# Performance work log

Hardware: AMD Instinct MI355X
Metric: run time of the kernel (lower is better)

## Reference

```python
import jax, jax.numpy as jnp
import numpy as np
import math

N_HEAD = 16
ROPE_BASE = 10000.0


def _rope(xh):
    # xh: [B, H, T, D]; rotate full head dim using half-split (GPT-NeoX style)
    B, H, T, D = xh.shape
    theta = 1.0 / (ROPE_BASE ** (jnp.arange(0, D, 2, dtype=jnp.float32) / D))  # [D/2]
    idx_theta = jnp.arange(T, dtype=jnp.float32)[:, None] * theta[None, :]      # [T, D/2]
    idx_theta2 = jnp.concatenate([idx_theta, idx_theta], axis=1)                 # [T, D]
    cos = jnp.cos(idx_theta2)[None, None]                                        # [1,1,T,D]
    sin = jnp.sin(idx_theta2)[None, None]
    d2 = D // 2
    neg_half = jnp.concatenate([-xh[..., d2:], xh[..., :d2]], axis=-1)
    return xh * cos + neg_half * sin


def setup_inputs() -> dict:
    key = jax.random.key(0)
    k1, k2, k3 = jax.random.split(key, 3)
    B, T, C = 2, 2048, 2048
    x = jax.random.normal(k1, (B, T, C), dtype=jnp.float32)
    w_attn = jax.random.normal(k2, (C, 3 * C), dtype=jnp.float32) * (1.0 / math.sqrt(C))
    w_proj = jax.random.normal(k3, (C, C), dtype=jnp.float32) * (1.0 / math.sqrt(C))
    return {"x": x, "w_attn": w_attn, "w_proj": w_proj}


def reference(x, w_attn, w_proj):
    B, T, C = x.shape
    H = N_HEAD
    D = C // H
    qkv = x @ w_attn                                   # [B,T,3C]
    q, k, v = jnp.split(qkv, 3, axis=-1)
    # [B,T,C] -> [B,H,T,D]
    to_heads = lambda t: t.reshape(B, T, H, D).transpose(0, 2, 1, 3)
    q, k, v = to_heads(q), to_heads(k), to_heads(v)
    q = _rope(q)
    k = _rope(k)
    att = jnp.einsum('bhqd,bhkd->bhqk', q, k) * (1.0 / math.sqrt(D))
    causal = jnp.tril(jnp.ones((T, T), dtype=bool))
    att = jnp.where(causal[None, None], att, -jnp.inf)
    att = jax.nn.softmax(att, axis=-1)
    y = jnp.einsum('bhqk,bhkd->bhqd', att, v)          # [B,H,T,D]
    y = y.transpose(0, 2, 1, 3).reshape(B, T, C)
    return y @ w_proj
```

## Files before the change

kernel.cpp:

```cpp
#include <hip/hip_runtime.h>
#include <hip/hip_bf16.h>
#include <math.h>

typedef __bf16 bf16;
typedef __bf16 bf16x8 __attribute__((ext_vector_type(8)));
typedef float f32x4 __attribute__((ext_vector_type(4)));
typedef float f32x16 __attribute__((ext_vector_type(16)));
typedef unsigned int u32x2 __attribute__((ext_vector_type(2)));
typedef unsigned int u32x4 __attribute__((ext_vector_type(4)));

#define MFMA16(a, b, c) __builtin_amdgcn_mfma_f32_16x16x32_bf16((a), (b), (c), 0, 0, 0)
#define MFMA32(a, b, c) __builtin_amdgcn_mfma_f32_32x32x16_bf16((a), (b), (c), 0, 0, 0)

static constexpr int Bsz = 2, Tsz = 2048, Csz = 2048, Hn = 16, Dh = 128;
static constexpr float ATTN_SCALE = 0.08838834764831845f;

__device__ __forceinline__ void gld16(const void* src, void* dst) {
    __builtin_amdgcn_global_load_lds((__attribute__((address_space(1))) void*)src,
                                     (__attribute__((address_space(3))) void*)dst,
                                     16, 0, 0);
}

__device__ __forceinline__ unsigned cvt_pk_bf16(float lo, float hi) {
    unsigned r;
    asm("v_cvt_pk_bf16_f32 %0, %1, %2" : "=v"(r) : "v"(lo), "v"(hi));
    return r;
}

__device__ __forceinline__ bf16x8 make_pfrag(float p0, float p1, float p2, float p3,
                                             float p4, float p5, float p6, float p7) {
    unsigned a0 = cvt_pk_bf16(p0, p1), a1 = cvt_pk_bf16(p2, p3);
    unsigned b0 = cvt_pk_bf16(p4, p5), b1 = cvt_pk_bf16(p6, p7);
    asm volatile("v_permlane32_swap_b32 %0, %1" : "+v"(a0), "+v"(b0));
    asm volatile("v_permlane32_swap_b32 %0, %1" : "+v"(a1), "+v"(b1));
    u32x4 w = {a0, a1, b0, b1};
    return __builtin_bit_cast(bf16x8, w);
}

__global__ __launch_bounds__(256) void cast_x_kernel(const float* __restrict__ x,
                                                     bf16* __restrict__ o, int n8) {
    int i = blockIdx.x * 256 + threadIdx.x;
    if (i >= n8) return;
    const float4* x4 = (const float4*)x;
    float4 a = x4[2 * i], b = x4[2 * i + 1];
    bf16x8 v;
    v[0] = (bf16)a.x; v[1] = (bf16)a.y; v[2] = (bf16)a.z; v[3] = (bf16)a.w;
    v[4] = (bf16)b.x; v[5] = (bf16)b.y; v[6] = (bf16)b.z; v[7] = (bf16)b.w;
    ((bf16x8*)o)[i] = v;
}

template <typename TIN>
__global__ __launch_bounds__(256) void transpose_cast_kernel(const TIN* __restrict__ in,
                                                             bf16* __restrict__ out,
                                                             int R, int Cc) {
    __shared__ float tile[64][65];
    const int tx = threadIdx.x, ty = threadIdx.y;
    in  += (size_t)blockIdx.z * R * Cc;
    out += (size_t)blockIdx.z * R * Cc;
    const int c0 = blockIdx.x * 64, r0 = blockIdx.y * 64;
#pragma unroll
    for (int j = 0; j < 16; ++j) {
        int rr = ty + j * 4;
        tile[rr][tx] = (float)in[(size_t)(r0 + rr) * Cc + c0 + tx];
    }
    __syncthreads();
#pragma unroll
    for (int j = 0; j < 16; ++j) {
        int cc = ty + j * 4;
        out[(size_t)(c0 + cc) * R + r0 + tx] = (bf16)tile[tx][cc];
    }
}

__global__ __launch_bounds__(256) void cossin_kernel(float2* __restrict__ cs) {
    int idx = blockIdx.x * 256 + threadIdx.x;
    int t = idx >> 6, i = idx & 63;
    float theta = 1.0f / powf(10000.0f, (float)(2 * i) / 128.0f);
    float ang = (float)t * theta;
    cs[idx] = make_float2(cosf(ang), sinf(ang));
}

__global__ __launch_bounds__(512, 2)
void gemm256_qkv(const bf16* __restrict__ A, const bf16* __restrict__ Bt,
                 bf16* __restrict__ Oq, bf16* __restrict__ Ok, bf16* __restrict__ Ov,
                 const float2* __restrict__ cs, int K) {
    __shared__ bf16 sA[2][256 * 64];
    __shared__ bf16 sB[2][256 * 64];
    const int tid = threadIdx.x, lane = tid & 63, wid = tid >> 6;
    const int wm = wid >> 2, wn = wid & 3;
    const int lo16 = lane & 15, hi4 = lane >> 4;

    const int cpx = gridDim.x >> 3;
    const int swz = (blockIdx.x & 7) * cpx + (blockIdx.x >> 3);
    const int by = swz & 15;
    const int bx = swz >> 4;
    const int row0 = by << 8, col0 = bx << 8;

    const int srow = tid >> 3;
    const int swzoff = (((tid & 7) ^ ((tid >> 3) & 7)) << 3);
    const bf16* srcA = A  + (size_t)(row0 + srow) * K + swzoff;
    const bf16* srcB = Bt + (size_t)(col0 + srow) * K + swzoff;
    const size_t K64 = (size_t)K * 64, K128 = (size_t)K * 128;
    char* const ldsA = (char*)&sA[0][0];
    char* const ldsB = (char*)&sB[0][0];
    const int wuo = wid << 10;

    auto issueA0 = [&](int c, int kt) {
        const bf16* s = srcA + (size_t)kt * 64;
        gld16(s,        ldsA + (c << 15) + 0     + wuo);
        gld16(s + K128, ldsA + (c << 15) + 16384 + wuo);
    };
    auto issueA1 = [&](int c, int kt) {
        const bf16* s = srcA + (size_t)kt * 64 + K64;
        gld16(s,        ldsA + (c << 15) + 8192  + wuo);
        gld16(s + K128, ldsA + (c << 15) + 24576 + wuo);
    };
    auto issueBlo = [&](int c, int kt) {
        const bf16* s = srcB + (size_t)kt * 64;
        gld16(s,       ldsB + (c << 15) + 0    + wuo);
        gld16(s + K64, ldsB + (c << 15) + 8192 + wuo);
    };
    auto issueBhi = [&](int c, int kt) {
        const bf16* s = srcB + (size_t)kt * 64 + K128;
        gld16(s,       ldsB + (c << 15) + 16384 + wuo);
        gld16(s + K64, ldsB + (c << 15) + 24576 + wuo);
    };
    auto ldF = [&](const char* buf, int row, int ks) {
        return *(const bf16x8*)(buf + row * 128 + ((((ks << 2) + hi4) ^ (row & 7)) << 4));
    };

    const int arow = (wm << 7) + lo16;
    const int brow = (wn << 4) + lo16;

    f32x4 acc[8][4] = {};
    const int nkt = K >> 6;

    issueBhi(0, 0); issueA1(0, 0); issueA0(0, 0); issueBlo(0, 0);
    if (nkt > 1) {
        issueA0(1, 1); issueBlo(1, 1);
        asm volatile("s_waitcnt vmcnt(4)" ::: "memory");
    } else {
        asm volatile("s_waitcnt vmcnt(0)" ::: "memory");
    }
    __builtin_amdgcn_s_barrier();

    for (int kt = 0; kt < nkt; ++kt) {
        const int c = kt & 1;
        const char* bufA = ldsA + (c << 15);
        const char* bufB = ldsB + (c << 15);
        bf16x8 af[4][2], bq[2][2];
#pragma unroll
        for (int i = 0; i < 4; ++i) {
            af[i][0] = ldF(bufA, arow + (i << 4), 0);
            af[i][1] = ldF(bufA, arow + (i << 4), 1);
        }
#pragma unroll
        for (int j = 0; j < 2; ++j) {
            bq[j][0] = ldF(bufB, brow + (j << 6), 0);
            bq[j][1] = ldF(bufB, brow + (j << 6), 1);
        }
        if (kt + 1 < nkt) issueBhi(c ^ 1, kt + 1);
        __builtin_amdgcn_s_barrier();
        asm volatile("s_waitcnt lgkmcnt(0)" ::: "memory");
        __builtin_amdgcn_sched_barrier(0);
        __builtin_amdgcn_s_setprio(1);
#pragma unroll
        for (int ks = 0; ks < 2; ++ks)
#pragma unroll
            for (int i = 0; i < 4; ++i)
#pragma unroll
                for (int j = 0; j < 2; ++j)
                    acc[i][j] = MFMA16(af[i][ks], bq[j][ks], acc[i][j]);
        __builtin_amdgcn_s_setprio(0);
        __builtin_amdgcn_s_barrier();
#pragma unroll
        for (int j = 0; j < 2; ++j) {
            bq[j][0] = ldF(bufB, brow + ((j + 2) << 6), 0);
            bq[j][1] = ldF(bufB, brow + ((j + 2) << 6), 1);
        }
        if (kt + 1 < nkt) issueA1(c ^ 1, kt + 1);
        __builtin_amdgcn_s_barrier();
        asm volatile("s_waitcnt lgkmcnt(0)" ::: "memory");
        __builtin_amdgcn_sched_barrier(0);
        __builtin_amdgcn_s_setprio(1);
#pragma unroll
        for (int ks = 0; ks < 2; ++ks)
#pragma unroll
            for (int i = 0; i < 4; ++i)
#pragma unroll
                for (int j = 0; j < 2; ++j)
                    acc[i][j + 2] = MFMA16(af[i][ks], bq[j][ks], acc[i][j + 2]);
        __builtin_amdgcn_s_setprio(0);
        __builtin_amdgcn_s_barrier();
#pragma unroll
        for (int i = 0; i < 4; ++i) {
            af[i][0] = ldF(bufA, arow + 64 + (i << 4), 0);
            af[i][1] = ldF(bufA, arow + 64 + (i << 4), 1);
        }
#pragma unroll
        for (int j = 0; j < 2; ++j) {
            bq[j][0] = ldF(bufB, brow + (j << 6), 0);
            bq[j][1] = ldF(bufB, brow + (j << 6), 1);
        }
        if (kt + 2 < nkt) issueA0(c, kt + 2);
        __builtin_amdgcn_s_barrier();
        asm volatile("s_waitcnt lgkmcnt(0)" ::: "memory");
        __builtin_amdgcn_sched_barrier(0);
        __builtin_amdgcn_s_setprio(1);
#pragma unroll
        for (int ks = 0; ks < 2; ++ks)
#pragma unroll
            for (int i = 0; i < 4; ++i)
#pragma unroll
                for (int j = 0; j < 2; ++j)
                    acc[i + 4][j] = MFMA16(af[i][ks], bq[j][ks], acc[i + 4][j]);
        __builtin_amdgcn_s_setprio(0);
        __builtin_amdgcn_s_barrier();
#pragma unroll
        for (int j = 0; j < 2; ++j) {
            bq[j][0] = ldF(bufB, brow + ((j + 2) << 6), 0);
            bq[j][1] = ldF(bufB, brow + ((j + 2) << 6), 1);
        }
        if (kt + 2 < nkt) issueBlo(c, kt + 2);
        __builtin_amdgcn_s_barrier();
        asm volatile("s_waitcnt lgkmcnt(0)" ::: "memory");
        __builtin_amdgcn_sched_barrier(0);
        __builtin_amdgcn_s_setprio(1);
#pragma unroll
        for (int ks = 0; ks < 2; ++ks)
#pragma unroll
            for (int i = 0; i < 4; ++i)
#pragma unroll
                for (int j = 0; j < 2; ++j)
                    acc[i + 4][j + 2] = MFMA16(af[i][ks], bq[j][ks], acc[i + 4][j + 2]);
        __builtin_amdgcn_s_setprio(0);
        if (kt + 2 < nkt) asm volatile("s_waitcnt vmcnt(4)" ::: "memory");
        else              asm volatile("s_waitcnt vmcnt(0)" ::: "memory");
        __builtin_amdgcn_s_barrier();
    }

    const int seg = col0 >> 11;
    const int hb = (col0 >> 7) & 15;
    if (seg < 2) {
        bf16* dst0 = (seg == 0) ? Oq : Ok;
        const float qs = (seg == 0) ? ATTN_SCALE : 1.0f;
        const int d = (wn << 4) + lo16;
#pragma unroll
        for (int mi = 0; mi < 8; ++mi)
#pragma unroll
            for (int r = 0; r < 4; ++r) {
                const int gm = row0 + (wm << 7) + (mi << 4) + (hi4 << 2) + r;
                const int b = gm >> 11, t = gm & 2047;
                const float2 csv = cs[t * 64 + d];
#pragma unroll
                for (int np = 0; np < 2; ++np) {
                    bf16* drow = dst0 + ((((size_t)b * Hn + hb + np) * Tsz + t) << 7);
                    const float vlo = acc[mi][2 * np][r];
                    const float vhi = acc[mi][2 * np + 1][r];
                    drow[d]      = (bf16)((vlo * csv.x - vhi * csv.y) * qs);
                    drow[d + 64] = (bf16)((vhi * csv.x + vlo * csv.y) * qs);
                }
            }
    } else {
        const int d0 = (wn << 4) + lo16;
#pragma unroll
        for (int mi = 0; mi < 8; ++mi)
#pragma unroll
            for (int r = 0; r < 4; ++r) {
                const int gm = row0 + (wm << 7) + (mi << 4) + (hi4 << 2) + r;
                const int b = gm >> 11, t = gm & 2047;
#pragma unroll
                for (int ni = 0; ni < 4; ++ni) {
                    bf16* drow = Ov + ((((size_t)b * Hn + hb + (ni >> 1)) * Tsz + t) << 7);
                    drow[d0 + ((ni & 1) << 6)] = (bf16)acc[mi][ni][r];
                }
            }
    }
}

__global__ __launch_bounds__(256)
void gemm128_bt(const bf16* __restrict__ A, const bf16* __restrict__ Bt,
                float* __restrict__ Cf, int M, int N, int K) {
    __shared__ bf16 sA[128 * 64];
    __shared__ bf16 sB[128 * 64];
    const int tid = threadIdx.x;
    const int lane = tid & 63, wv = tid >> 6;
    const int wr = wv >> 1, wc = wv & 1;
    const int lo16 = lane & 15, hi4 = lane >> 4;
    const int row0 = blockIdx.y << 7, col0 = blockIdx.x << 7;

    f32x4 acc[4][4] = {};

    const int nkt = K >> 6;
    for (int kt = 0; kt < nkt; ++kt) {
        const int kbase = kt << 6;
#pragma unroll
        for (int c = 0; c < 4; ++c) {
            const int o16 = (c << 8) + tid;
            const int row = o16 >> 3, u = o16 & 7;
            const int colel = kbase + ((u ^ (row & 7)) << 3);
            gld16(A  + (size_t)(row0 + row) * K + colel,
                  (char*)sA + (((c << 8) + (wv << 6)) << 4));
            gld16(Bt + (size_t)(col0 + row) * K + colel,
                  (char*)sB + (((c << 8) + (wv << 6)) << 4));
        }
        __syncthreads();
#pragma unroll
        for (int ks = 0; ks < 2; ++ks) {
            bf16x8 af[4], bfv[4];
#pragma unroll
            for (int mi = 0; mi < 4; ++mi) {
                const int ar = (wr << 6) + (mi << 4) + lo16;
                af[mi] = *(const bf16x8*)((const char*)sA + ar * 128 +
                          (((ks << 6) + (hi4 << 4)) ^ ((ar & 7) << 4)));
            }
#pragma unroll
            for (int ni = 0; ni < 4; ++ni) {
                const int bc = (wc << 4) + (ni << 5) + lo16;
                bfv[ni] = *(const bf16x8*)((const char*)sB + bc * 128 +
                           (((ks << 6) + (hi4 << 4)) ^ ((bc & 7) << 4)));
            }
#pragma unroll
            for (int mi = 0; mi < 4; ++mi)
#pragma unroll
                for (int ni = 0; ni < 4; ++ni)
                    acc[mi][ni] = MFMA16(af[mi], bfv[ni], acc[mi][ni]);
        }
        __syncthreads();
    }

#pragma unroll
    for (int mi = 0; mi < 4; ++mi)
#pragma unroll
        for (int r = 0; r < 4; ++r) {
            const int gm = row0 + (wr << 6) + (mi << 4) + (hi4 << 2) + r;
            float* crow = Cf + (size_t)gm * N + col0 + (wc << 4) + lo16;
#pragma unroll
            for (int ni = 0; ni < 4; ++ni)
                crow[ni << 5] = acc[mi][ni][r];
        }
}

__device__ __forceinline__ void stage_tile(const bf16* __restrict__ Kb,
                                           const bf16* __restrict__ Vtb,
                                           bf16* sKc, bf16* sVc, int k0, int tid) {
#pragma unroll
    for (int c = 0; c < 4; ++c) {
        const int off = (c << 12) + (tid << 4);
        const int row = off >> 8, u = (off >> 4) & 15;
        gld16(Kb + (size_t)(k0 + row) * Dh + ((u ^ (row & 7)) << 3), (char*)sKc + off);
        const int dv = off >> 7, uv = (off >> 4) & 7;
        gld16(Vtb + (size_t)dv * Tsz + k0 + ((uv ^ (dv & 7)) << 3), (char*)sVc + off);
    }
}

__global__ __launch_bounds__(256, 2)
void attn_kernel(const bf16* __restrict__ Q, const bf16* __restrict__ K,
                 const bf16* __restrict__ Vt, bf16* __restrict__ Y) {
    __shared__ bf16 sK[2][64 * 128];
    __shared__ bf16 sV[2][128 * 64];
    const int tid = threadIdx.x, lane = tid & 63, wv = tid >> 6;
    const int lo32 = lane & 31, hl = lane >> 5;

    const int i = blockIdx.x;
    const int g = i >> 5;
    const int bh = i & 31;
    const int t = (i < 256) ? (15 - g) : (g - 8);
    const int b = bh >> 4, h = bh & 15;

    const int q0 = t << 7;
    const int q0w = q0 + (wv << 5);
    const int qg = q0w + lo32;

    const bf16* Kb  = K  + (size_t)bh * (Tsz * Dh);
    const bf16* Vtb = Vt + (size_t)bh * (Tsz * Dh);
    const bf16* Qp  = Q  + (size_t)bh * (Tsz * Dh) + (size_t)qg * Dh;

    bf16x8 qf[8];
#pragma unroll
    for (int kc = 0; kc < 8; ++kc)
        qf[kc] = *(const bf16x8*)(Qp + (kc << 4) + (hl << 3));

    float m = -1e30f, lsum = 0.f;
    f32x16 o[4] = {};

    const int nt_block = 2 * t + 2;
    const int nt_warp = ((q0w + 31) >> 6) + 1;

    stage_tile(Kb, Vtb, &sK[0][0], &sV[0][0], 0, tid);

    int cur = 0;
    for (int kt = 0; kt < nt_block; ++kt) {
        __syncthreads();
        if (kt + 1 < nt_block)
            stage_tile(Kb, Vtb, &sK[cur ^ 1][0], &sV[cur ^ 1][0], (kt + 1) << 6, tid);
        if (kt < nt_warp) {
            const int k0 = kt << 6;
            const bf16* kbuf = &sK[cur][0];
            const bf16* vbuf = &sV[cur][0];
            f32x16 s0 = {}, s1 = {};
            const int swk = lo32 & 7;
            __builtin_amdgcn_s_setprio(1);
#pragma unroll
            for (int kc = 0; kc < 8; ++kc) {
                bf16x8 kf0 = *(const bf16x8*)((const char*)kbuf + lo32 * 256 +
                              ((((kc << 1) + hl) ^ swk) << 4));
                s0 = MFMA32(kf0, qf[kc], s0);
                bf16x8 kf1 = *(const bf16x8*)((const char*)kbuf + (32 + lo32) * 256 +
                              ((((kc << 1) + hl) ^ swk) << 4));
                s1 = MFMA32(kf1, qf[kc], s1);
            }
            __builtin_amdgcn_s_setprio(0);

            const bool bnd = (k0 + 63 > q0w);
            if (bnd) {
#pragma unroll
                for (int r = 0; r < 16; ++r) {
                    const int kl = (r & 3) + ((r >> 2) << 3) + (hl << 2);
                    if (k0 + kl > qg)      s0[r] = -1e30f;
                    if (k0 + 32 + kl > qg) s1[r] = -1e30f;
                }
            }
            float pm = s0[0];
#pragma unroll
            for (int r = 1; r < 16; ++r) pm = fmaxf(pm, s0[r]);
#pragma unroll
            for (int r = 0; r < 16; ++r) pm = fmaxf(pm, s1[r]);
            pm = fmaxf(pm, __shfl_xor(pm, 32));

            if (__any(pm > m + 8.0f)) {
                const float mn = fmaxf(m, pm);
                const float sc = __expf(m - mn);
                m = mn;
                lsum *= sc;
#pragma unroll
                for (int db = 0; db < 4; ++db)
#pragma unroll
                    for (int r = 0; r < 16; ++r) o[db][r] *= sc;
            }
            float rs = 0.f;
            if (bnd) {
#pragma unroll
                for (int r = 0; r < 16; ++r) {
                    float e0 = (s0[r] > -1e29f) ? __expf(s0[r] - m) : 0.f;
                    float e1 = (s1[r] > -1e29f) ? __expf(s1[r] - m) : 0.f;
                    s0[r] = e0; s1[r] = e1; rs += e0 + e1;
                }
            } else {
#pragma unroll
                for (int r = 0; r < 16; ++r) {
                    float e0 = __expf(s0[r] - m);
                    float e1 = __expf(s1[r] - m);
                    s0[r] = e0; s1[r] = e1; rs += e0 + e1;
                }
            }
            rs += __shfl_xor(rs, 32);
            lsum += rs;

            bf16x8 pb0 = make_pfrag(s0[0], s0[1], s0[2],  s0[3],  s0[4],  s0[5],  s0[6],  s0[7]);
            bf16x8 pb1 = make_pfrag(s0[8], s0[9], s0[10], s0[11], s0[12], s0[13], s0[14], s0[15]);
            bf16x8 pb2 = make_pfrag(s1[0], s1[1], s1[2],  s1[3],  s1[4],  s1[5],  s1[6],  s1[7]);
            bf16x8 pb3 = make_pfrag(s1[8], s1[9], s1[10], s1[11], s1[12], s1[13], s1[14], s1[15]);

            __builtin_amdgcn_s_setprio(1);
#pragma unroll
            for (int db = 0; db < 4; ++db) {
                const int rd = (db << 5) + lo32;
                const char* vrow = (const char*)vbuf + rd * 128;
                const int sw = rd & 7;
                bf16x8 v0 = *(const bf16x8*)(vrow + (((0 + hl) ^ sw) << 4));
                o[db] = MFMA32(v0, pb0, o[db]);
                bf16x8 v1 = *(const bf16x8*)(vrow + (((2 + hl) ^ sw) << 4));
                o[db] = MFMA32(v1, pb1, o[db]);
                bf16x8 v2 = *(const bf16x8*)(vrow + (((4 + hl) ^ sw) << 4));
                o[db] = MFMA32(v2, pb2, o[db]);
                bf16x8 v3 = *(const bf16x8*)(vrow + (((6 + hl) ^ sw) << 4));
                o[db] = MFMA32(v3, pb3, o[db]);
            }
            __builtin_amdgcn_s_setprio(0);
        }
        cur ^= 1;
    }

    const float inv = 1.0f / lsum;
    const size_t rowoff = ((size_t)b * Tsz + qg) * (size_t)Csz + (size_t)h * 128;
#pragma unroll
    for (int db = 0; db < 4; ++db)
#pragma unroll
        for (int gg = 0; gg < 4; ++gg) {
            unsigned w0 = cvt_pk_bf16(o[db][4 * gg + 0] * inv, o[db][4 * gg + 1] * inv);
            unsigned w1 = cvt_pk_bf16(o[db][4 * gg + 2] * inv, o[db][4 * gg + 3] * inv);
            u32x2 w = {w0, w1};
            *(u32x2*)(Y + rowoff + (db << 5) + (gg << 3) + (hl << 2)) = w;
        }
}

extern "C" void kernel_launch(void* const* d_in, const int* in_sizes, int n_in,
                              void* d_out, int out_size, void* d_ws, size_t ws_size,
                              hipStream_t stream) {
    const float* x      = (const float*)d_in[0];
    const float* w_attn = (const float*)d_in[1];
    const float* w_proj = (const float*)d_in[2];
    float* out = (float*)d_out;

    char* ws = (char*)d_ws;
    bf16* Xb  = (bf16*)(ws);
    bf16* Wat = (bf16*)(ws + 16777216);
    bf16* Wpt = (bf16*)(ws + 41943040);
    bf16* Qr  = (bf16*)(ws + 50331648);
    bf16* Kr  = (bf16*)(ws + 67108864);
    bf16* Vb  = (bf16*)(ws + 83886080);
    bf16* Vt  = (bf16*)(ws + 100663296);
    bf16* Yb  = (bf16*)(ws + 117440512);
    float2* cs = (float2*)(ws + 134217728);

    cast_x_kernel<<<4096, 256, 0, stream>>>(x, Xb, (Bsz * Tsz * Csz) / 8);
    transpose_cast_kernel<float><<<dim3(96, 32, 1), dim3(64, 4), 0, stream>>>(w_attn, Wat, 2048, 6144);
    transpose_cast_kernel<float><<<dim3(32, 32, 1), dim3(64, 4), 0, stream>>>(w_proj, Wpt, 2048, 2048);
    cossin_kernel<<<512, 256, 0, stream>>>(cs);

    gemm256_qkv<<<384, 512, 0, stream>>>(Xb, Wat, Qr, Kr, Vb, cs, 2048);
    transpose_cast_kernel<bf16><<<dim3(2, 32, 32), dim3(64, 4), 0, stream>>>(Vb, Vt, 2048, 128);

    attn_kernel<<<dim3(512), 256, 0, stream>>>(Qr, Kr, Vt, Yb);

    gemm128_bt<<<dim3(16, 32), 256, 0, stream>>>(Yb, Wpt, out, 4096, 2048, 2048);
}
```

Before: 273.2 us.

## Load all A fragments once per k-tile and reorder prefetch stages in QKV GEMM

The GEMM main loop now reads all eight A row-fragments from LDS once per k-tile and holds them in registers. Each of the four MFMA phases then loads only one B column-fragment, where before A was reloaded halfway through and B fragments were re-read. The global-to-LDS prefetch order is reshuffled to match: A0/A1 for tile kt+1 are issued up front, B halves for the next tile come in phases 1-2, and A halves for kt+2 in phases 3-4. The aim is fewer LDS reads per tile, at the cost of more live VGPRs for A fragments and a changed wait/barrier pattern that could hurt occupancy or introduce hazards.

Result: no change. 272.3 us (-0.3%).

```diff
diff --git a/kernel.cpp b/kernel.cpp
--- a/kernel.cpp
+++ b/kernel.cpp
@@ -136,7 +136,7 @@
 
     issueBhi(0, 0); issueA1(0, 0); issueA0(0, 0); issueBlo(0, 0);
     if (nkt > 1) {
-        issueA0(1, 1); issueBlo(1, 1);
+        issueA0(1, 1); issueA1(1, 1);
         asm volatile("s_waitcnt vmcnt(4)" ::: "memory");
     } else {
         asm volatile("s_waitcnt vmcnt(0)" ::: "memory");
@@ -147,17 +147,14 @@
         const int c = kt & 1;
         const char* bufA = ldsA + (c << 15);
         const char* bufB = ldsB + (c << 15);
-        bf16x8 af[4][2], bq[2][2];
-#pragma unroll
-        for (int i = 0; i < 4; ++i) {
+        bf16x8 af[8][2], bq[2];
+#pragma unroll
+        for (int i = 0; i < 8; ++i) {
             af[i][0] = ldF(bufA, arow + (i << 4), 0);
             af[i][1] = ldF(bufA, arow + (i << 4), 1);
         }
-#pragma unroll
-        for (int j = 0; j < 2; ++j) {
-            bq[j][0] = ldF(bufB, brow + (j << 6), 0);
-            bq[j][1] = ldF(bufB, brow + (j << 6), 1);
-        }
+        bq[0] = ldF(bufB, brow, 0);
+        bq[1] = ldF(bufB, brow, 1);
         if (kt + 1 < nkt) issueBhi(c ^ 1, kt + 1);
         __builtin_amdgcn_s_barrier();
         asm volatile("s_waitcnt lgkmcnt(0)" ::: "memory");
@@ -166,18 +163,13 @@
 #pragma unroll
         for (int ks = 0; ks < 2; ++ks)
 #pragma unroll
-            for (int i = 0; i < 4; ++i)
-#pragma unroll
-                for (int j = 0; j < 2; ++j)
-                    acc[i][j] = MFMA16(af[i][ks], bq[j][ks], acc[i][j]);
+            for (int i = 0; i < 8; ++i)
+                acc[i][0] = MFMA16(af[i][ks], bq[ks], acc[i][0]);
         __builtin_amdgcn_s_setprio(0);
         __builtin_amdgcn_s_barrier();
-#pragma unroll
-        for (int j = 0; j < 2; ++j) {
-            bq[j][0] = ldF(bufB, brow + ((j + 2) << 6), 0);
-            bq[j][1] = ldF(bufB, brow + ((j + 2) << 6), 1);
-        }
-        if (kt + 1 < nkt) issueA1(c ^ 1, kt + 1);
+        bq[0] = ldF(bufB, brow + 64, 0);
+        bq[1] = ldF(bufB, brow + 64, 1);
+        if (kt + 1 < nkt) issueBlo(c ^ 1, kt + 1);
         __builtin_amdgcn_s_barrier();
         asm volatile("s_waitcnt lgkmcnt(0)" ::: "memory");
         __builtin_amdgcn_sched_barrier(0);
@@ -185,22 +177,12 @@
 #pragma unroll
         for (int ks = 0; ks < 2; ++ks)
 #pragma unroll
-            for (int i = 0; i < 4; ++i)
-#pragma unroll
-                for (int j = 0; j < 2; ++j)
-                    acc[i][j + 2] = MFMA16(af[i][ks], bq[j][ks], acc[i][j + 2]);
+            for (int i = 0; i < 8; ++i)
+                acc[i][1] = MFMA16(af[i][ks], bq[ks], acc[i][1]);
         __builtin_amdgcn_s_setprio(0);
         __builtin_amdgcn_s_barrier();
-#pragma unroll
-        for (int i = 0; i < 4; ++i) {
-            af[i][0] = ldF(bufA, arow + 64 + (i << 4), 0);
-            af[i][1] = ldF(bufA, arow + 64 + (i << 4), 1);
-        }
-#pragma unroll
-        for (int j = 0; j < 2; ++j) {
-            bq[j][0] = ldF(bufB, brow + (j << 6), 0);
-            bq[j][1] = ldF(bufB, brow + (j << 6), 1);
-        }
+        bq[0] = ldF(bufB, brow + 128, 0);
+        bq[1] = ldF(bufB, brow + 128, 1);
         if (kt + 2 < nkt) issueA0(c, kt + 2);
         __builtin_amdgcn_s_barrier();
         asm volatile("s_waitcnt lgkmcnt(0)" ::: "memory");
@@ -209,18 +191,13 @@
 #pragma unroll
         for (int ks = 0; ks < 2; ++ks)
 #pragma unroll
-            for (int i = 0; i < 4; ++i)
-#pragma unroll
-                for (int j = 0; j < 2; ++j)
-                    acc[i + 4][j] = MFMA16(af[i][ks], bq[j][ks], acc[i + 4][j]);
+            for (int i = 0; i < 8; ++i)
+                acc[i][2] = MFMA16(af[i][ks], bq[ks], acc[i][2]);
         __builtin_amdgcn_s_setprio(0);
         __builtin_amdgcn_s_barrier();
-#pragma unroll
-        for (int j = 0; j < 2; ++j) {
-            bq[j][0] = ldF(bufB, brow + ((j + 2) << 6), 0);
-            bq[j][1] = ldF(bufB, brow + ((j + 2) << 6), 1);
-        }
-        if (kt + 2 < nkt) issueBlo(c, kt + 2);
+        bq[0] = ldF(bufB, brow + 192, 0);
+        bq[1] = ldF(bufB, brow + 192, 1);
+        if (kt + 2 < nkt) issueA1(c, kt + 2);
         __builtin_amdgcn_s_barrier();
         asm volatile("s_waitcnt lgkmcnt(0)" ::: "memory");
         __builtin_amdgcn_sched_barrier(0);
@@ -228,13 +205,11 @@
 #pragma unroll
         for (int ks = 0; ks < 2; ++ks)
 #pragma unroll
-            for (int i = 0; i < 4; ++i)
-#pragma unroll
-                for (int j = 0; j < 2; ++j)
-                    acc[i + 4][j + 2] = MFMA16(af[i][ks], bq[j][ks], acc[i + 4][j + 2]);
+            for (int i = 0; i < 8; ++i)
+                acc[i][3] = MFMA16(af[i][ks], bq[ks], acc[i][3]);
         __builtin_amdgcn_s_setprio(0);
-        if (kt + 2 < nkt) asm volatile("s_waitcnt vmcnt(4)" ::: "memory");
-        else              asm volatile("s_waitcnt vmcnt(0)" ::: "memory");
+        if (kt + 2 < nkt)      asm volatile("s_waitcnt vmcnt(4)" ::: "memory");
+        else if (kt + 1 < nkt) asm volatile("s_waitcnt vmcnt(0)" ::: "memory");
         __builtin_amdgcn_s_barrier();
     }
 
```
